# Kernel tuning notes

Measured on AMD Instinct MI355X. Metric: run time of the kernel, lower is better.

Reference implementation:

```python
import jax, jax.numpy as jnp
import numpy as np
from jax import lax

# Module constants (from init_kwargs)
K = 1.0            # conductivity
H = 1.0 / 1023.0   # grid spacing
VALUE = 0.0        # Dirichlet boundary value
STENCIL = np.array([[0.0, 0.25, 0.0],
                    [0.25, 0.0, 0.25],
                    [0.0, 0.25, 0.0]], dtype=np.float32)


def setup_inputs() -> dict:
    key = jax.random.key(0)
    k1, k2 = jax.random.split(key)
    B, C, Hn, Wn = 16, 1, 1024, 1024
    u = jax.random.normal(k1, (B, C, Hn, Wn), dtype=jnp.float32)
    f = jax.random.normal(k2, (B, C, Hn, Wn), dtype=jnp.float32)
    # conv weight: (out=1, in=1, 3, 3), repeated over in_channels (=1 here)
    weight = jnp.asarray(STENCIL).reshape(1, 1, 3, 3)
    return {"u": u, "f": f, "weight": weight}


def reference(u, f, weight):
    # v = detached interior of u, padded with the Dirichlet value
    v_int = lax.stop_gradient(u[..., 1:-1, 1:-1])           # [B,1,H-2,W-2]
    v = jnp.pad(v_int, ((0, 0), (0, 0), (1, 1), (1, 1)),
                mode="constant", constant_values=VALUE)      # [B,1,H,W]
    # 5-point Jacobi stencil, VALID conv -> interior shape [B,1,H-2,W-2]
    conv = lax.conv_general_dilated(
        v, weight, window_strides=(1, 1), padding="VALID",
        dimension_numbers=("NCHW", "OIHW", "NCHW"))
    cof = -(H ** 2) / (K * 4.0)
    source = lax.stop_gradient((cof * f)[..., 1:-1, 1:-1])
    # interior <- stencil(v) + source; boundary stays at Dirichlet VALUE
    out = v.at[..., 1:-1, 1:-1].set(conv + source)
    return out
```

## Files before the change

kernel.cpp:

```cpp
#include <hip/hip_runtime.h>

#define IMG_W 1024
#define IMG_H 1024

__global__ __launch_bounds__(256) void dir_rhs_kernel(
    const float* __restrict__ u,
    const float* __restrict__ f,
    const float* __restrict__ wt,
    float* __restrict__ out)
{
    const int row = blockIdx.x;
    const int b   = row >> 10;
    const int i   = row & (IMG_H - 1);
    const int tid = threadIdx.x;
    const int j0  = tid << 2;
    const size_t img = (size_t)b << 20;

    float4* out4 = (float4*)(out + img + (size_t)i * IMG_W + j0);

    if (i == 0 || i == IMG_H - 1) {
        *out4 = make_float4(0.f, 0.f, 0.f, 0.f);
        return;
    }

    const float w00 = wt[0], w01 = wt[1], w02 = wt[2];
    const float w10 = wt[3], w11 = wt[4], w12 = wt[5];
    const float w20 = wt[6], w21 = wt[7], w22 = wt[8];
    const float cof = (float)(-(1.0 / 1023.0) * (1.0 / 1023.0) / 4.0);

    const float* urow = u + img + (size_t)i * IMG_W;

    float vm[6], vc[6], vp[6];

    const bool left_edge  = (j0 == 0);
    const bool right_edge = (j0 + 4 >= IMG_W);

    {
        float4 c = *(const float4*)(urow + j0);
        vc[1] = c.x; vc[2] = c.y; vc[3] = c.z; vc[4] = c.w;
        vc[0] = left_edge  ? 0.f : urow[j0 - 1];
        vc[5] = right_edge ? 0.f : urow[j0 + 4];
        if (left_edge)  vc[1] = 0.f;
        if (right_edge) vc[4] = 0.f;
    }
    if (i == 1) {
        #pragma unroll
        for (int k = 0; k < 6; k++) vm[k] = 0.f;
    } else {
        const float* r = urow - IMG_W;
        float4 c = *(const float4*)(r + j0);
        vm[1] = c.x; vm[2] = c.y; vm[3] = c.z; vm[4] = c.w;
        vm[0] = left_edge  ? 0.f : r[j0 - 1];
        vm[5] = right_edge ? 0.f : r[j0 + 4];
        if (left_edge)  vm[1] = 0.f;
        if (right_edge) vm[4] = 0.f;
    }
    if (i == IMG_H - 2) {
        #pragma unroll
        for (int k = 0; k < 6; k++) vp[k] = 0.f;
    } else {
        const float* r = urow + IMG_W;
        float4 c = *(const float4*)(r + j0);
        vp[1] = c.x; vp[2] = c.y; vp[3] = c.z; vp[4] = c.w;
        vp[0] = left_edge  ? 0.f : r[j0 - 1];
        vp[5] = right_edge ? 0.f : r[j0 + 4];
        if (left_edge)  vp[1] = 0.f;
        if (right_edge) vp[4] = 0.f;
    }

    float4 f4 = *(const float4*)(f + img + (size_t)i * IMG_W + j0);
    float ff[4] = {f4.x, f4.y, f4.z, f4.w};

    float res[4];
    #pragma unroll
    for (int e = 0; e < 4; e++) {
        float acc = cof * ff[e];
        acc += w00 * vm[e] + w01 * vm[e + 1] + w02 * vm[e + 2];
        acc += w10 * vc[e] + w11 * vc[e + 1] + w12 * vc[e + 2];
        acc += w20 * vp[e] + w21 * vp[e + 1] + w22 * vp[e + 2];
        res[e] = acc;
    }
    if (left_edge)  res[0] = 0.f;
    if (right_edge) res[3] = 0.f;

    *out4 = make_float4(res[0], res[1], res[2], res[3]);
}

extern "C" void kernel_launch(void* const* d_in, const int* in_sizes, int n_in,
                              void* d_out, int out_size, void* d_ws, size_t ws_size,
                              hipStream_t stream) {
    const float* u  = (const float*)d_in[0];
    const float* f  = (const float*)d_in[1];
    const float* wt = (const float*)d_in[2];
    float* out = (float*)d_out;

    const int B = 16;
    dim3 grid(B * IMG_H);
    dim3 block(256);
    dir_rhs_kernel<<<grid, block, 0, stream>>>(u, f, wt, out);
}
```

Measured before the change: 167.4 us.

## Process eight rows per block with register row-rolling and nontemporal stores

Each block now handles 8 consecutive rows of one image instead of a single row. It keeps three rows of u in registers and rolls them forward, so each u row is loaded about once rather than three times. Output writes use nontemporal stores to avoid polluting the cache. The grid shrinks 8x, which reduces parallelism per block count and adds serial latency per thread in exchange for less redundant load traffic.

```diff
diff --git a/kernel.cpp b/kernel.cpp
--- a/kernel.cpp
+++ b/kernel.cpp
@@ -2,6 +2,9 @@
 
 #define IMG_W 1024
 #define IMG_H 1024
+#define ROWS  8
+
+typedef float v4f __attribute__((ext_vector_type(4)));
 
 __global__ __launch_bounds__(256) void dir_rhs_kernel(
     const float* __restrict__ u,
@@ -9,81 +12,80 @@
     const float* __restrict__ wt,
     float* __restrict__ out)
 {
-    const int row = blockIdx.x;
-    const int b   = row >> 10;
-    const int i   = row & (IMG_H - 1);
-    const int tid = threadIdx.x;
-    const int j0  = tid << 2;
+    const int tile = blockIdx.x;
+    const int b    = tile >> 7;
+    const int r0   = (tile & 127) << 3;
+    const int tid  = threadIdx.x;
+    const int j0   = tid << 2;
     const size_t img = (size_t)b << 20;
 
-    float4* out4 = (float4*)(out + img + (size_t)i * IMG_W + j0);
+    const float* ub = u   + img;
+    const float* fb = f   + img;
+    float*       ob = out + img;
 
-    if (i == 0 || i == IMG_H - 1) {
-        *out4 = make_float4(0.f, 0.f, 0.f, 0.f);
-        return;
-    }
+    const bool le = (j0 == 0);
+    const bool re = (j0 + 4 >= IMG_W);
 
     const float w00 = wt[0], w01 = wt[1], w02 = wt[2];
     const float w10 = wt[3], w11 = wt[4], w12 = wt[5];
     const float w20 = wt[6], w21 = wt[7], w22 = wt[8];
     const float cof = (float)(-(1.0 / 1023.0) * (1.0 / 1023.0) / 4.0);
 
-    const float* urow = u + img + (size_t)i * IMG_W;
+    float vm[6], vc[6], vp[6], nx[6];
 
-    float vm[6], vc[6], vp[6];
+    auto loadv = [&](float* a, int r) {
+        if (r < 1 || r > IMG_H - 2) {
+            #pragma unroll
+            for (int q = 0; q < 6; q++) a[q] = 0.f;
+            return;
+        }
+        const float* p = ub + (size_t)r * IMG_W;
+        v4f c = *(const v4f*)(p + j0);
+        a[1] = c.x; a[2] = c.y; a[3] = c.z; a[4] = c.w;
+        a[0] = le ? 0.f : p[j0 - 1];
+        a[5] = re ? 0.f : p[j0 + 4];
+        if (le) a[1] = 0.f;
+        if (re) a[4] = 0.f;
+    };
 
-    const bool left_edge  = (j0 == 0);
-    const bool right_edge = (j0 + 4 >= IMG_W);
+    loadv(vm, r0 - 1);
+    loadv(vc, r0);
+    loadv(vp, r0 + 1);
 
-    {
-        float4 c = *(const float4*)(urow + j0);
-        vc[1] = c.x; vc[2] = c.y; vc[3] = c.z; vc[4] = c.w;
-        vc[0] = left_edge  ? 0.f : urow[j0 - 1];
-        vc[5] = right_edge ? 0.f : urow[j0 + 4];
-        if (left_edge)  vc[1] = 0.f;
-        if (right_edge) vc[4] = 0.f;
+    #pragma unroll
+    for (int k = 0; k < ROWS; k++) {
+        const int r = r0 + k;
+
+        loadv(nx, r + 2);
+
+        v4f* o4 = (v4f*)(ob + (size_t)r * IMG_W + j0);
+
+        if (r == 0 || r == IMG_H - 1) {
+            v4f z = {0.f, 0.f, 0.f, 0.f};
+            __builtin_nontemporal_store(z, o4);
+        } else {
+            v4f f4 = *(const v4f*)(fb + (size_t)r * IMG_W + j0);
+            float ff[4] = {f4.x, f4.y, f4.z, f4.w};
+
+            float res[4];
+            #pragma unroll
+            for (int e = 0; e < 4; e++) {
+                float acc = cof * ff[e];
+                acc += w00 * vm[e] + w01 * vm[e + 1] + w02 * vm[e + 2];
+                acc += w10 * vc[e] + w11 * vc[e + 1] + w12 * vc[e + 2];
+                acc += w20 * vp[e] + w21 * vp[e + 1] + w22 * vp[e + 2];
+                res[e] = acc;
+            }
+            if (le) res[0] = 0.f;
+            if (re) res[3] = 0.f;
+
+            v4f rv = {res[0], res[1], res[2], res[3]};
+            __builtin_nontemporal_store(rv, o4);
+        }
+
+        #pragma unroll
+        for (int q = 0; q < 6; q++) { vm[q] = vc[q]; vc[q] = vp[q]; vp[q] = nx[q]; }
     }
-    if (i == 1) {
-        #pragma unroll
-        for (int k = 0; k < 6; k++) vm[k] = 0.f;
-    } else {
-        const float* r = urow - IMG_W;
-        float4 c = *(const float4*)(r + j0);
-        vm[1] = c.x; vm[2] = c.y; vm[3] = c.z; vm[4] = c.w;
-        vm[0] = left_edge  ? 0.f : r[j0 - 1];
-        vm[5] = right_edge ? 0.f : r[j0 + 4];
-        if (left_edge)  vm[1] = 0.f;
-        if (right_edge) vm[4] = 0.f;
-    }
-    if (i == IMG_H - 2) {
-        #pragma unroll
-        for (int k = 0; k < 6; k++) vp[k] = 0.f;
-    } else {
-        const float* r = urow + IMG_W;
-        float4 c = *(const float4*)(r + j0);
-        vp[1] = c.x; vp[2] = c.y; vp[3] = c.z; vp[4] = c.w;
-        vp[0] = left_edge  ? 0.f : r[j0 - 1];
-        vp[5] = right_edge ? 0.f : r[j0 + 4];
-        if (left_edge)  vp[1] = 0.f;
-        if (right_edge) vp[4] = 0.f;
-    }
-
-    float4 f4 = *(const float4*)(f + img + (size_t)i * IMG_W + j0);
-    float ff[4] = {f4.x, f4.y, f4.z, f4.w};
-
-    float res[4];
-    #pragma unroll
-    for (int e = 0; e < 4; e++) {
-        float acc = cof * ff[e];
-        acc += w00 * vm[e] + w01 * vm[e + 1] + w02 * vm[e + 2];
-        acc += w10 * vc[e] + w11 * vc[e + 1] + w12 * vc[e + 2];
-        acc += w20 * vp[e] + w21 * vp[e + 1] + w22 * vp[e + 2];
-        res[e] = acc;
-    }
-    if (left_edge)  res[0] = 0.f;
-    if (right_edge) res[3] = 0.f;
-
-    *out4 = make_float4(res[0], res[1], res[2], res[3]);
 }
 
 extern "C" void kernel_launch(void* const* d_in, const int* in_sizes, int n_in,
@@ -95,7 +97,7 @@
     float* out = (float*)d_out;
 
     const int B = 16;
-    dim3 grid(B * IMG_H);
+    dim3 grid(B * (IMG_H / ROWS));
     dim3 block(256);
     dir_rhs_kernel<<<grid, block, 0, stream>>>(u, f, wt, out);
 }
```

Result: slower. 174.4 us (+4.2%).
